# Kernel tuning notes

Measured on AMD Instinct MI355X. Metric: run time of the kernel, lower is better.

Reference implementation:

```python
import jax, jax.numpy as jnp
import numpy as np

N_NODES = 10000
N_EDGES = 160000
NF = 512  # node_features
DIMS = [1, 2 * NF // 8, 4 * NF // 8, NF]  # 1 -> 128 -> 256 -> 512


def setup_inputs() -> dict:
    key = jax.random.key(0)
    ks = jax.random.split(key, 10)
    inp = {
        "x": jax.random.normal(ks[0], (N_NODES, 1), dtype=jnp.float32),
        "edge_index": jax.random.randint(ks[1], (2, N_EDGES), 0, N_NODES, dtype=jnp.int64),
        "edge_weights": jax.random.uniform(ks[2], (N_EDGES,), dtype=jnp.float32),
    }
    # Glorot-style init for GCNConv linear weights, zero biases (PyG default)
    for i in range(3):
        d_in, d_out = DIMS[i], DIMS[i + 1]
        scale = (6.0 / (d_in + d_out)) ** 0.5
        inp[f"W{i+1}"] = jax.random.uniform(ks[3 + i], (d_in, d_out), dtype=jnp.float32, minval=-scale, maxval=scale)
        inp[f"b{i+1}"] = jnp.zeros((d_out,), dtype=jnp.float32)
    return inp


def _gcn_layer(h, W, b, src, dst, ew):
    # GCNConv with add_self_loops=False, normalize=False:
    #   h' = scatter_sum(edge_weight * (h @ W)[src] -> dst) + b
    h = h @ W                                    # [N, d_out]
    msg = h[src] * ew[:, None]                   # [E, d_out] gather + scale
    agg = jax.ops.segment_sum(msg, dst, num_segments=N_NODES)  # scatter-add
    return agg + b


def reference(x, edge_index, edge_weights, W1, b1, W2, b2, W3, b3):
    src, dst = edge_index[0], edge_index[1]  # source_to_target flow
    h = _gcn_layer(x, W1, b1, src, dst, edge_weights)
    h = _gcn_layer(h, W2, b2, src, dst, edge_weights)
    h = _gcn_layer(h, W3, b3, src, dst, edge_weights)
    return jax.nn.sigmoid(h)
```

## Files before the change

### kernel.cpp

```cpp
#include <hip/hip_runtime.h>
#include <math.h>

#define N_NODES 10000
#define N_EDGES 160000
#define CAP 64


__global__ __launch_bounds__(512) void k0_kernel(
        int* __restrict__ cnt, float* __restrict__ sdf,
        const float* __restrict__ W1, const float* __restrict__ b1,
        const float* __restrict__ W2,
        float* __restrict__ u_part, float* __restrict__ v_part) {
    int tid = threadIdx.x;
    int blk = blockIdx.x;
    if (blk == 0) {
        for (int g = tid; g < N_NODES / 4; g += 512)
            ((int4*)cnt)[g] = make_int4(0, 0, 0, 0);
    } else if (blk == 1) {
        for (int g = tid; g < 2 * N_NODES / 4; g += 512)
            ((float4*)sdf)[g] = make_float4(0.f, 0.f, 0.f, 0.f);
    } else {
        int b = blk - 2;
        if (tid < 256) {
            int j0 = b * 8;
            float uu = 0.f, vv = 0.f;
            #pragma unroll
            for (int jj = 0; jj < 8; ++jj) {
                float w2 = W2[(j0 + jj) * 256 + tid];
                uu = fmaf(W1[j0 + jj], w2, uu);
                vv = fmaf(b1[j0 + jj], w2, vv);
            }
            u_part[b * 256 + tid] = uu;
            v_part[b * 256 + tid] = vv;
        }
    }
}

__global__ __launch_bounds__(512) void k1_kernel(
        const int* __restrict__ src, const int* __restrict__ dst,
        const float* __restrict__ ew, const float* __restrict__ x,
        int* __restrict__ cnt, float2* __restrict__ bucket,
        float* __restrict__ sdf,
        const float* __restrict__ u_part, const float* __restrict__ v_part,
        const float* __restrict__ b2, const float* __restrict__ W3,
        float* __restrict__ p_part, float* __restrict__ q_part,
        float* __restrict__ r_part) {
    int tid = threadIdx.x;
    int blk = blockIdx.x;
    if (blk < 313) {
        int e = blk * 512 + tid;
        if (e < N_EDGES) {
            int   s = src[e];
            int   d = dst[e];
            float w = ew[e];
            float xs = x[s];
            int slot = atomicAdd(&cnt[d], 1);
            if (slot < CAP)
                bucket[d * CAP + slot] = make_float2(__int_as_float(s), w);
            atomicAdd(&sdf[2 * d],     w * xs);
            atomicAdd(&sdf[2 * d + 1], w);
        }
    } else {
        int c = blk - 313;
        __shared__ float su[16], sv[16], sb[16];
        if (tid < 16) {
            int kk = c * 16 + tid;
            float uu = 0.f, vv = 0.f;
            #pragma unroll
            for (int b = 0; b < 16; ++b) {
                uu += u_part[b * 256 + kk];
                vv += v_part[b * 256 + kk];
            }
            su[tid] = uu; sv[tid] = vv; sb[tid] = b2[kk];
        }
        __syncthreads();
        float pp = 0.f, qq = 0.f, rr = 0.f;
        #pragma unroll
        for (int kk = 0; kk < 16; ++kk) {
            float w3 = W3[(c * 16 + kk) * 512 + tid];
            pp = fmaf(su[kk], w3, pp);
            qq = fmaf(sv[kk], w3, qq);
            rr = fmaf(sb[kk], w3, rr);
        }
        p_part[c * 512 + tid] = pp;
        q_part[c * 512 + tid] = qq;
        r_part[c * 512 + tid] = rr;
    }
}

__global__ __launch_bounds__(512) void k2_kernel(
        const int* __restrict__ cnt, const float2* __restrict__ bucket,
        const float2* __restrict__ sd,
        float* __restrict__ t2, float* __restrict__ Bf,
        const float* __restrict__ p_part, const float* __restrict__ q_part,
        const float* __restrict__ r_part,
        float* __restrict__ p, float* __restrict__ q, float* __restrict__ r) {
    int tid = threadIdx.x;
    int blk = blockIdx.x;
    if (blk < 313) {
        int gid = blk * 512 + tid;
        int n = gid >> 4;
        int l = gid & 15;
        if (n < N_NODES) {
            int c = cnt[n]; if (c > CAP) c = CAP;
            float tt = 0.f, bb = 0.f;
            for (int i = l; i < c; i += 16) {
                float2 e = bucket[n * CAP + i];
                float2 v = sd[__float_as_int(e.x)];
                tt = fmaf(e.y, v.x, tt);
                bb = fmaf(e.y, v.y, bb);
            }
            #pragma unroll
            for (int m = 1; m < 16; m <<= 1) {
                tt += __shfl_xor(tt, m);
                bb += __shfl_xor(bb, m);
            }
            if (l == 0) { t2[n] = tt; Bf[n] = bb; }
        }
    } else {
        float pp = 0.f, qq = 0.f, rr = 0.f;
        #pragma unroll
        for (int c2 = 0; c2 < 16; ++c2) {
            pp += p_part[c2 * 512 + tid];
            qq += q_part[c2 * 512 + tid];
            rr += r_part[c2 * 512 + tid];
        }
        p[tid] = pp; q[tid] = qq; r[tid] = rr;
    }
}

__global__ __launch_bounds__(256) void output_kernel(
        const int* __restrict__ cnt, const float2* __restrict__ bucket,
        const float* __restrict__ t2, const float* __restrict__ Bf,
        const float2* __restrict__ sd,
        const float* __restrict__ p, const float* __restrict__ q,
        const float* __restrict__ r, const float* __restrict__ b3,
        float* __restrict__ out) {
    int tid = threadIdx.x;
    int n0 = blockIdx.x * 16;
    __shared__ float A_l[16], B_l[16], D_l[16];
    {
        int nl = tid >> 4;
        int l = tid & 15;
        int n = n0 + nl;
        int c = cnt[n]; if (c > CAP) c = CAP;
        float acc = 0.f;
        for (int i = l; i < c; i += 16) {
            float2 e = bucket[n * CAP + i];
            acc = fmaf(e.y, t2[__float_as_int(e.x)], acc);
        }
        #pragma unroll
        for (int m = 1; m < 16; m <<= 1) acc += __shfl_xor(acc, m);
        if (l == 0) {
            A_l[nl] = acc;
            B_l[nl] = Bf[n];
            D_l[nl] = sd[n].y;
        }
    }
    __syncthreads();
    #pragma unroll
    for (int h = 0; h < 8; ++h) {
        int idx = h * 256 + tid;
        int nl = idx >> 7;
        int j = idx & 127;
        float a = A_l[nl], b = B_l[nl], dg = D_l[nl];
        float4 P = ((const float4*)p)[j];
        float4 Q = ((const float4*)q)[j];
        float4 R = ((const float4*)r)[j];
        float4 B3 = ((const float4*)b3)[j];
        float4 o;
        float zx = fmaf(a, P.x, fmaf(b, Q.x, fmaf(dg, R.x, B3.x)));
        float zy = fmaf(a, P.y, fmaf(b, Q.y, fmaf(dg, R.y, B3.y)));
        float zz = fmaf(a, P.z, fmaf(b, Q.z, fmaf(dg, R.z, B3.z)));
        float zw = fmaf(a, P.w, fmaf(b, Q.w, fmaf(dg, R.w, B3.w)));
        o.x = 1.f / (1.f + __expf(-zx));
        o.y = 1.f / (1.f + __expf(-zy));
        o.z = 1.f / (1.f + __expf(-zz));
        o.w = 1.f / (1.f + __expf(-zw));
        ((float4*)out)[(size_t)(n0 + nl) * 128 + j] = o;
    }
}

extern "C" void kernel_launch(void* const* d_in, const int* in_sizes, int n_in,
                              void* d_out, int out_size, void* d_ws, size_t ws_size,
                              hipStream_t stream) {
    const float* x  = (const float*)d_in[0];
    const int*   ei = (const int*)d_in[1];
    const float* ew = (const float*)d_in[2];
    const float* W1 = (const float*)d_in[3];
    const float* b1 = (const float*)d_in[4];
    const float* W2 = (const float*)d_in[5];
    const float* b2 = (const float*)d_in[6];
    const float* W3 = (const float*)d_in[7];
    const float* b3 = (const float*)d_in[8];
    float* out = (float*)d_out;

    float* ws       = (float*)d_ws;
    int*    cnt     = (int*)ws;
    float*  sdf     = ws + 10240;
    float2* sd      = (float2*)sdf;
    float*  t2      = ws + 30240;
    float*  Bf      = ws + 40240;
    float*  p       = ws + 50240;
    float*  q       = ws + 50752;
    float*  r       = ws + 51264;
    float*  u_part  = ws + 51776;
    float*  v_part  = ws + 55872;
    float*  p_part  = ws + 60000;
    float*  q_part  = ws + 68192;
    float*  r_part  = ws + 76384;
    float2* bucket  = (float2*)(ws + 84576);

    const int* src = ei;
    const int* dst = ei + N_EDGES;

    k0_kernel<<<18, 512, 0, stream>>>(cnt, sdf, W1, b1, W2, u_part, v_part);
    k1_kernel<<<329, 512, 0, stream>>>(src, dst, ew, x, cnt, bucket, sdf,
                                       u_part, v_part, b2, W3,
                                       p_part, q_part, r_part);
    k2_kernel<<<314, 512, 0, stream>>>(cnt, bucket, sd, t2, Bf,
                                       p_part, q_part, r_part, p, q, r);
    output_kernel<<<625, 256, 0, stream>>>(cnt, bucket, t2, Bf, sd,
                                           p, q, r, b3, out);
}
```

Before: 116.7 us.

## Replace float atomics for layer-1 sums with two-hop bucket gather in k2

```diff
diff --git a/kernel.cpp b/kernel.cpp
--- a/kernel.cpp
+++ b/kernel.cpp
@@ -7,7 +7,7 @@
 
 
 __global__ __launch_bounds__(512) void k0_kernel(
-        int* __restrict__ cnt, float* __restrict__ sdf,
+        int* __restrict__ cnt,
         const float* __restrict__ W1, const float* __restrict__ b1,
         const float* __restrict__ W2,
         float* __restrict__ u_part, float* __restrict__ v_part) {
@@ -16,11 +16,8 @@
     if (blk == 0) {
         for (int g = tid; g < N_NODES / 4; g += 512)
             ((int4*)cnt)[g] = make_int4(0, 0, 0, 0);
-    } else if (blk == 1) {
-        for (int g = tid; g < 2 * N_NODES / 4; g += 512)
-            ((float4*)sdf)[g] = make_float4(0.f, 0.f, 0.f, 0.f);
     } else {
-        int b = blk - 2;
+        int b = blk - 1;
         if (tid < 256) {
             int j0 = b * 8;
             float uu = 0.f, vv = 0.f;
@@ -38,9 +35,8 @@
 
 __global__ __launch_bounds__(512) void k1_kernel(
         const int* __restrict__ src, const int* __restrict__ dst,
-        const float* __restrict__ ew, const float* __restrict__ x,
+        const float* __restrict__ ew,
         int* __restrict__ cnt, float2* __restrict__ bucket,
-        float* __restrict__ sdf,
         const float* __restrict__ u_part, const float* __restrict__ v_part,
         const float* __restrict__ b2, const float* __restrict__ W3,
         float* __restrict__ p_part, float* __restrict__ q_part,
@@ -53,12 +49,9 @@
             int   s = src[e];
             int   d = dst[e];
             float w = ew[e];
-            float xs = x[s];
             int slot = atomicAdd(&cnt[d], 1);
             if (slot < CAP)
                 bucket[d * CAP + slot] = make_float2(__int_as_float(s), w);
-            atomicAdd(&sdf[2 * d],     w * xs);
-            atomicAdd(&sdf[2 * d + 1], w);
         }
     } else {
         int c = blk - 313;
@@ -90,8 +83,8 @@
 
 __global__ __launch_bounds__(512) void k2_kernel(
         const int* __restrict__ cnt, const float2* __restrict__ bucket,
-        const float2* __restrict__ sd,
-        float* __restrict__ t2, float* __restrict__ Bf,
+        const float* __restrict__ x,
+        float* __restrict__ t2, float2* __restrict__ bd,
         const float* __restrict__ p_part, const float* __restrict__ q_part,
         const float* __restrict__ r_part,
         float* __restrict__ p, float* __restrict__ q, float* __restrict__ r) {
@@ -102,20 +95,35 @@
         int n = gid >> 4;
         int l = gid & 15;
         if (n < N_NODES) {
-            int c = cnt[n]; if (c > CAP) c = CAP;
-            float tt = 0.f, bb = 0.f;
-            for (int i = l; i < c; i += 16) {
+            int cn = cnt[n]; if (cn > CAP) cn = CAP;
+            float t2a = 0.f, bfa = 0.f, dga = 0.f;
+            for (int i = l; i < cn; i += 16) {
                 float2 e = bucket[n * CAP + i];
-                float2 v = sd[__float_as_int(e.x)];
-                tt = fmaf(e.y, v.x, tt);
-                bb = fmaf(e.y, v.y, bb);
+                int   s = __float_as_int(e.x);
+                float w = e.y;
+                dga += w;
+                int cs = cnt[s]; if (cs > CAP) cs = CAP;
+                const float2* bs = &bucket[s * CAP];
+                float s1 = 0.f, dgs = 0.f;
+                #pragma unroll 4
+                for (int j = 0; j < cs; ++j) {
+                    float2 e2 = bs[j];
+                    s1 = fmaf(e2.y, x[__float_as_int(e2.x)], s1);
+                    dgs += e2.y;
+                }
+                t2a = fmaf(w, s1, t2a);
+                bfa = fmaf(w, dgs, bfa);
             }
             #pragma unroll
             for (int m = 1; m < 16; m <<= 1) {
-                tt += __shfl_xor(tt, m);
-                bb += __shfl_xor(bb, m);
-            }
-            if (l == 0) { t2[n] = tt; Bf[n] = bb; }
+                t2a += __shfl_xor(t2a, m);
+                bfa += __shfl_xor(bfa, m);
+                dga += __shfl_xor(dga, m);
+            }
+            if (l == 0) {
+                t2[n] = t2a;
+                bd[n] = make_float2(bfa, dga);
+            }
         }
     } else {
         float pp = 0.f, qq = 0.f, rr = 0.f;
@@ -131,8 +139,7 @@
 
 __global__ __launch_bounds__(256) void output_kernel(
         const int* __restrict__ cnt, const float2* __restrict__ bucket,
-        const float* __restrict__ t2, const float* __restrict__ Bf,
-        const float2* __restrict__ sd,
+        const float* __restrict__ t2, const float2* __restrict__ bd,
         const float* __restrict__ p, const float* __restrict__ q,
         const float* __restrict__ r, const float* __restrict__ b3,
         float* __restrict__ out) {
@@ -152,9 +159,10 @@
         #pragma unroll
         for (int m = 1; m < 16; m <<= 1) acc += __shfl_xor(acc, m);
         if (l == 0) {
+            float2 v = bd[n];
             A_l[nl] = acc;
-            B_l[nl] = Bf[n];
-            D_l[nl] = sd[n].y;
+            B_l[nl] = v.x;
+            D_l[nl] = v.y;
         }
     }
     __syncthreads();
@@ -197,29 +205,27 @@
 
     float* ws       = (float*)d_ws;
     int*    cnt     = (int*)ws;
-    float*  sdf     = ws + 10240;
-    float2* sd      = (float2*)sdf;
-    float*  t2      = ws + 30240;
-    float*  Bf      = ws + 40240;
-    float*  p       = ws + 50240;
-    float*  q       = ws + 50752;
-    float*  r       = ws + 51264;
-    float*  u_part  = ws + 51776;
-    float*  v_part  = ws + 55872;
-    float*  p_part  = ws + 60000;
-    float*  q_part  = ws + 68192;
-    float*  r_part  = ws + 76384;
-    float2* bucket  = (float2*)(ws + 84576);
+    float*  t2      = ws + 10240;
+    float2* bd      = (float2*)(ws + 20240);
+    float*  p       = ws + 40240;
+    float*  q       = ws + 40752;
+    float*  r       = ws + 41264;
+    float*  u_part  = ws + 41776;
+    float*  v_part  = ws + 45872;
+    float*  p_part  = ws + 50000;
+    float*  q_part  = ws + 58192;
+    float*  r_part  = ws + 66384;
+    float2* bucket  = (float2*)(ws + 74576);
 
     const int* src = ei;
     const int* dst = ei + N_EDGES;
 
-    k0_kernel<<<18, 512, 0, stream>>>(cnt, sdf, W1, b1, W2, u_part, v_part);
-    k1_kernel<<<329, 512, 0, stream>>>(src, dst, ew, x, cnt, bucket, sdf,
+    k0_kernel<<<17, 512, 0, stream>>>(cnt, W1, b1, W2, u_part, v_part);
+    k1_kernel<<<329, 512, 0, stream>>>(src, dst, ew, cnt, bucket,
                                        u_part, v_part, b2, W3,
                                        p_part, q_part, r_part);
-    k2_kernel<<<314, 512, 0, stream>>>(cnt, bucket, sd, t2, Bf,
+    k2_kernel<<<314, 512, 0, stream>>>(cnt, bucket, x, t2, bd,
                                        p_part, q_part, r_part, p, q, r);
-    output_kernel<<<625, 256, 0, stream>>>(cnt, bucket, t2, Bf, sd,
+    output_kernel<<<625, 256, 0, stream>>>(cnt, bucket, t2, bd,
                                            p, q, r, b3, out);
 }
```

Result: slower. 119.3 us (+2.3%).
